# Optimization experiments

Hardware: AMD Instinct MI355X
Metric: run time of the kernel (lower is better)

Reference implementation:

```python
import jax, jax.numpy as jnp
import numpy as np

B, N, H, D = 4, 2048, 16, 64
FEATS = H * D  # 1024; module scales scores by sqrt(feats), not sqrt(head_dim)


def setup_inputs() -> dict:
    key = jax.random.key(0)
    ks = jax.random.split(key, 9)
    s = 1.0 / np.sqrt(D)
    return {
        "x": jax.random.normal(ks[0], (B, N, H, D), dtype=jnp.float32),
        "Wq": jax.random.uniform(ks[1], (H, D, D), jnp.float32, -s, s),
        "bq": jax.random.uniform(ks[2], (H, D), jnp.float32, -s, s),
        "Wk": jax.random.uniform(ks[3], (H, D, D), jnp.float32, -s, s),
        "bk": jax.random.uniform(ks[4], (H, D), jnp.float32, -s, s),
        "Wv": jax.random.uniform(ks[5], (H, D, D), jnp.float32, -s, s),
        "bv": jax.random.uniform(ks[6], (H, D), jnp.float32, -s, s),
        "Wo": jax.random.uniform(ks[7], (H, D, D), jnp.float32, -s, s),
        "bo": jax.random.uniform(ks[8], (H, D), jnp.float32, -s, s),
    }


def reference(x, Wq, bq, Wk, bk, Wv, bv, Wo, bo):
    # per-head linears as one batched einsum: [b,n,h,d] x [h,d,o] -> [b,n,h,o]
    q = jnp.einsum("bnhd,hdo->bnho", x, Wq) + bq
    k = jnp.einsum("bnhd,hdo->bnho", x, Wk) + bk
    v = jnp.einsum("bnhd,hdo->bnho", x, Wv) + bv
    sqrt_d = jnp.asarray(FEATS, x.dtype) ** 0.5  # sqrt(feats) per original code
    # scores: [b,h,i,j]
    score = jax.nn.softmax(jnp.einsum("bihf,bjhf->bhij", q, k) / sqrt_d, axis=-1)
    attn = jnp.einsum("bhij,bjhf->bihf", score, v)  # [b,n,h,d]
    out = jnp.einsum("bnhd,hdo->bnho", attn, Wo) + bo
    return out
```

## Files before the change

kernel.cpp:

```cpp
#include <hip/hip_runtime.h>

#define Bsz  4
#define Nseq 2048
#define Hn   16
#define Dh   64
#define BH   (Bsz*Hn)
#define NT64 (Nseq/64)
#define NT32 (Nseq/32)

#define AS1 __attribute__((address_space(1)))
#define AS3 __attribute__((address_space(3)))

typedef __attribute__((ext_vector_type(8))) short bf16x8;
typedef __attribute__((ext_vector_type(16))) float f32x16;
typedef __attribute__((ext_vector_type(4))) float f32x4;
typedef __attribute__((ext_vector_type(2))) float f32x2;
typedef __attribute__((ext_vector_type(4))) unsigned short u16x4;

#define MFMA32 __builtin_amdgcn_mfma_f32_32x32x16_bf16

static __device__ __forceinline__ unsigned short f2bf(float f) {
    unsigned u = __float_as_uint(f);
    u = (u + 0x7fffu + ((u >> 16) & 1u)) >> 16;
    return (unsigned short)u;
}
static __device__ __forceinline__ float bf2f(unsigned short s) {
    return __uint_as_float((unsigned)s << 16);
}
static __device__ __forceinline__ unsigned cvt_pk_bf16(float lo, float hi) {
    unsigned r;
    asm("v_cvt_pk_bf16_f32 %0, %1, %2" : "=v"(r) : "v"(lo), "v"(hi));
    return r;
}
static __device__ __forceinline__ void swap32(unsigned &a, unsigned &b) {
    asm("v_permlane32_swap_b32 %0, %1" : "+v"(a), "+v"(b));
}
static __device__ __forceinline__ float exp2v(float x) {
    float r;
    asm("v_exp_f32 %0, %1" : "=v"(r) : "v"(x));
    return r;
}
static __device__ __forceinline__ f32x2 pk_add(f32x2 a, f32x2 b) {
    f32x2 d;
    asm("v_pk_add_f32 %0, %1, %2" : "=v"(d) : "v"(a), "v"(b));
    return d;
}

__global__ __launch_bounds__(256) void wprep_kernel(
    const float* __restrict__ Wq, const float* __restrict__ Wk,
    const float* __restrict__ Wv,
    unsigned short* __restrict__ gWtH, unsigned short* __restrict__ gWtL)
{
    __shared__ float ws[64][65];
    const int mh = blockIdx.x;
    const int m = mh >> 4, h = mh & 15;
    const int tid = threadIdx.x;
    const float* W = (m == 0 ? Wq : (m == 1 ? Wk : Wv)) + h * 4096;

    for (int c = tid; c < 1024; c += 256) {
        int row = c >> 4, col = (c & 15) * 4;
        *(f32x4*)&ws[row][col] = *(const f32x4*)&W[row * 64 + col];
    }
    __syncthreads();

    const int o = tid >> 2, dblk = (tid & 3) * 16;
    size_t base = ((size_t)mh * 64 + o) * 64 + dblk;
#pragma unroll
    for (int i4 = 0; i4 < 4; ++i4) {
        u16x4 vh, vl;
#pragma unroll
        for (int j = 0; j < 4; ++j) {
            float v = ws[dblk + i4 * 4 + j][o];
            unsigned short hh = f2bf(v);
            vh[j] = hh;
            vl[j] = f2bf(v - bf2f(hh));
        }
        *(u16x4*)&gWtH[base + i4 * 4] = vh;
        *(u16x4*)&gWtL[base + i4 * 4] = vl;
    }
}

__global__ __launch_bounds__(256) void proj_kernel(
    const float* __restrict__ x,
    const unsigned short* __restrict__ gWtH, const unsigned short* __restrict__ gWtL,
    const float* __restrict__ bq, const float* __restrict__ bk,
    const float* __restrict__ bv,
    unsigned short* __restrict__ gQ, unsigned short* __restrict__ gK,
    unsigned short* __restrict__ gVt)
{
    const int bh = blockIdx.x, h = bh & (Hn - 1), b = bh >> 4;
    const int n0 = blockIdx.y * 64;
    const int tid = threadIdx.x;
    const int w = tid >> 6, lane = tid & 63, l31 = lane & 31, l5 = lane >> 5;
    const int qi = w >> 1, oj = w & 1;

    const int nrow = n0 + qi * 32 + l31;
    const float* xrow = x + (((size_t)b * Nseq + nrow) * Hn + h) * Dh;

    bf16x8 xh[4], xl[4];
#pragma unroll
    for (int ks = 0; ks < 4; ++ks) {
        f32x4 v0 = *(const f32x4*)&xrow[ks * 16 + l5 * 8];
        f32x4 v1 = *(const f32x4*)&xrow[ks * 16 + l5 * 8 + 4];
#pragma unroll
        for (int e = 0; e < 4; ++e) {
            unsigned short h0 = f2bf(v0[e]);
            xh[ks][e] = (short)h0;
            xl[ks][e] = (short)f2bf(v0[e] - bf2f(h0));
            unsigned short h1 = f2bf(v1[e]);
            xh[ks][4 + e] = (short)h1;
            xl[ks][4 + e] = (short)f2bf(v1[e] - bf2f(h1));
        }
    }

    const int o = oj * 32 + l31;

    f32x16 acc[3] = {};
#pragma unroll
    for (int m = 0; m < 3; ++m) {
        const unsigned short* WH = gWtH + (((size_t)m * 16 + h) * 64 + o) * 64;
        const unsigned short* WL = gWtL + (((size_t)m * 16 + h) * 64 + o) * 64;
#pragma unroll
        for (int ks = 0; ks < 4; ++ks) {
            bf16x8 wh = *(const bf16x8*)&WH[ks * 16 + l5 * 8];
            bf16x8 wl = *(const bf16x8*)&WL[ks * 16 + l5 * 8];
            if (m < 2) {
                acc[m] = MFMA32(xh[ks], wh, acc[m], 0, 0, 0);
                acc[m] = MFMA32(xl[ks], wh, acc[m], 0, 0, 0);
                acc[m] = MFMA32(xh[ks], wl, acc[m], 0, 0, 0);
            } else {
                acc[2] = MFMA32(wh, xh[ks], acc[2], 0, 0, 0);
                acc[2] = MFMA32(wl, xh[ks], acc[2], 0, 0, 0);
                acc[2] = MFMA32(wh, xl[ks], acc[2], 0, 0, 0);
            }
        }
    }

    {
        float bias = bq[h * 64 + o];
#pragma unroll
        for (int r = 0; r < 16; ++r) {
            int nl = (r & 3) + 8 * (r >> 2) + 4 * l5;
            int n = n0 + qi * 32 + nl;
            gQ[((size_t)bh * Nseq + n) * Dh + o] =
                f2bf((acc[0][r] + bias) * 0.0450842200f);
        }
    }
    {
        float bias = bk[h * 64 + o];
#pragma unroll
        for (int r = 0; r < 16; ++r) {
            int nl = (r & 3) + 8 * (r >> 2) + 4 * l5;
            int n = n0 + qi * 32 + nl;
            int c = (((o >> 3) ^ (n & 7)) * 8) + (o & 7);
            gK[((size_t)bh * Nseq + n) * Dh + c] = f2bf(acc[1][r] + bias);
        }
    }
    {
        const int tile = (n0 >> 5) + qi;
        const int kt = l31;
#pragma unroll
        for (int r = 0; r < 16; ++r) {
            int ol = (r & 3) + 8 * (r >> 2) + 4 * l5;
            int ov = oj * 32 + ol;
            float bias = bv[h * 64 + ov];
            int c = (((kt >> 3) ^ ((ov >> 2) & 3)) * 8) + (kt & 7);
            gVt[(((size_t)bh * NT32 + tile) * 64 + ov) * 32 + c] =
                f2bf(acc[2][r] + bias);
        }
    }
}

__global__ __launch_bounds__(256, 4) void flash_kernel(
    const unsigned short* __restrict__ gQ,
    const unsigned short* __restrict__ gK,
    const unsigned short* __restrict__ gVt,
    const float* __restrict__ Wo, const float* __restrict__ bo,
    float* __restrict__ out)
{
    __shared__ unsigned short kbuf[2][4096];
    __shared__ unsigned short vbuf[2][4096];

    const int bh = blockIdx.x, h = bh & (Hn - 1), b = bh >> 4;
    const int tid = threadIdx.x;
    const int w = tid >> 6, lane = tid & 63;
    const int l31 = lane & 31, l5 = lane >> 5;
    const int qrow = blockIdx.y * 128 + w * 32 + l31;

    bf16x8 qf[4];
#pragma unroll
    for (int kk = 0; kk < 4; ++kk)
        qf[kk] = *(const bf16x8*)&gQ[((size_t)bh * Nseq + qrow) * Dh + kk * 16 + l5 * 8];

    float z0 = 0.f;
    asm volatile("" : "+v"(z0));
    f32x16 zc = {z0, z0, z0, z0, z0, z0, z0, z0, z0, z0, z0, z0, z0, z0, z0, z0};

    f32x16 acc[2] = {};
    float l = 0.f;

    auto stage = [&](int t, int bufi) {
        const unsigned short* ks = gK + ((size_t)bh * Nseq + (size_t)t * 64) * Dh;
        const unsigned short* vs = gVt + ((size_t)(bh * NT32 + 2 * t)) * 2048;
#pragma unroll
        for (int i = 0; i < 2; ++i) {
            int off = w * 1024 + i * 512 + lane * 8;
            __builtin_amdgcn_global_load_lds((const AS1 void*)(ks + off),
                                             (AS3 void*)(&kbuf[bufi][w * 1024 + i * 512]), 16, 0, 0);
            __builtin_amdgcn_global_load_lds((const AS1 void*)(vs + off),
                                             (AS3 void*)(&vbuf[bufi][w * 1024 + i * 512]), 16, 0, 0);
        }
    };

    auto qk_tile = [&](const unsigned short* __restrict__ kb) -> f32x16 {
        const int roff = l31 * 64;
        const int sw = l31 & 7;
        bf16x8 kf = *(const bf16x8*)&kb[roff + ((l5 ^ sw) * 8)];
        f32x16 s = MFMA32(kf, qf[0], zc, 0, 0, 0);
#pragma unroll
        for (int kk = 1; kk < 4; ++kk) {
            kf = *(const bf16x8*)&kb[roff + (((kk * 2 + l5) ^ sw) * 8)];
            s = MFMA32(kf, qf[kk], s, 0, 0, 0);
        }
        return s;
    };

    auto soft_pv = [&](f32x16& s, const unsigned short* __restrict__ vb) {
#pragma unroll
        for (int r = 0; r < 16; ++r) s[r] = exp2v(s[r]);
        f32x2* sp = (f32x2*)&s;
        f32x2 u0 = pk_add(sp[0], sp[1]), u1 = pk_add(sp[2], sp[3]);
        f32x2 u2 = pk_add(sp[4], sp[5]), u3 = pk_add(sp[6], sp[7]);
        u0 = pk_add(u0, u1); u2 = pk_add(u2, u3);
        u0 = pk_add(u0, u2);
        l += u0[0] + u0[1];
#pragma unroll
        for (int ks = 0; ks < 2; ++ks) {
            const int b0 = 8 * ks;
            unsigned x0 = cvt_pk_bf16(s[b0 + 0], s[b0 + 1]);
            unsigned x1 = cvt_pk_bf16(s[b0 + 2], s[b0 + 3]);
            unsigned y0 = cvt_pk_bf16(s[b0 + 4], s[b0 + 5]);
            unsigned y1 = cvt_pk_bf16(s[b0 + 6], s[b0 + 7]);
            swap32(x0, y0);
            swap32(x1, y1);
            bf16x8 pf;
            ((unsigned*)&pf)[0] = x0; ((unsigned*)&pf)[1] = x1;
            ((unsigned*)&pf)[2] = y0; ((unsigned*)&pf)[3] = y1;
#pragma unroll
            for (int dt = 0; dt < 2; ++dt) {
                const int row = dt * 32 + l31;
                bf16x8 vf = *(const bf16x8*)&vb[row * 32 + (((ks * 2 + l5) ^ ((row >> 2) & 3)) * 8)];
                acc[dt] = MFMA32(vf, pf, acc[dt], 0, 0, 0);
            }
        }
    };

    auto window_step = [&](const unsigned short* __restrict__ kb,
                           const unsigned short* __restrict__ vb) {
        f32x16 sA = qk_tile(kb);
        f32x16 sB = qk_tile(kb + 2048);
        soft_pv(sA, vb);
        soft_pv(sB, vb + 2048);
    };

    stage(0, 0);

#pragma unroll 1
    for (int t2 = 0; t2 < NT64; t2 += 2) {
        __syncthreads();
        stage(t2 + 1, 1);
        window_step(&kbuf[0][0], &vbuf[0][0]);
        __syncthreads();
        if (t2 + 2 < NT64) stage(t2 + 2, 0);
        window_step(&kbuf[1][0], &vbuf[1][0]);
    }

    __syncthreads();
    {
        unsigned short* wl = &kbuf[0][0];
        for (int c = tid; c < 512; c += 256) {
            int o = c >> 3, c8 = c & 7;
            int cc = ((c8 ^ (o & 7)) * 8);
#pragma unroll
            for (int jj = 0; jj < 4; ++jj) wl[o * 64 + cc + jj]     = f2bf(Wo[(h * 64 + c8 * 8 + jj) * 64 + o]);
#pragma unroll
            for (int jj = 0; jj < 4; ++jj) wl[o * 64 + cc + 4 + jj] = f2bf(Wo[(h * 64 + c8 * 8 + 4 + jj) * 64 + o]);
        }
    }
    __syncthreads();

    l += __shfl_xor(l, 32);
    float inv = 1.f / l;
#pragma unroll
    for (int dt = 0; dt < 2; ++dt)
#pragma unroll
        for (int r = 0; r < 16; ++r) acc[dt][r] *= inv;

    const unsigned short* wot = &kbuf[0][0];
    f32x16 oc[2] = {};
#pragma unroll
    for (int kk = 0; kk < 4; ++kk) {
        const int dt = kk >> 1;
        const int b0 = 8 * (kk & 1);
        unsigned x0 = cvt_pk_bf16(acc[dt][b0 + 0], acc[dt][b0 + 1]);
        unsigned x1 = cvt_pk_bf16(acc[dt][b0 + 2], acc[dt][b0 + 3]);
        unsigned y0 = cvt_pk_bf16(acc[dt][b0 + 4], acc[dt][b0 + 5]);
        unsigned y1 = cvt_pk_bf16(acc[dt][b0 + 6], acc[dt][b0 + 7]);
        swap32(x0, y0);
        swap32(x1, y1);
        bf16x8 af;
        ((unsigned*)&af)[0] = x0; ((unsigned*)&af)[1] = x1;
        ((unsigned*)&af)[2] = y0; ((unsigned*)&af)[3] = y1;
#pragma unroll
        for (int ot = 0; ot < 2; ++ot) {
            int row = ot * 32 + l31;
            bf16x8 wf = *(const bf16x8*)&wot[row * 64 + (((kk * 2 + l5) ^ (row & 7)) * 8)];
            oc[ot] = MFMA32(wf, af, oc[ot], 0, 0, 0);
        }
    }

    float* obase = out + (((size_t)b * Nseq + qrow) * Hn + h) * Dh;
#pragma unroll
    for (int ot = 0; ot < 2; ++ot)
#pragma unroll
        for (int rq = 0; rq < 4; ++rq) {
            int o = ot * 32 + rq * 8 + l5 * 4;
            f32x4 bb = *(const f32x4*)&bo[h * 64 + o];
            f32x4 vv;
            vv[0] = oc[ot][rq * 4 + 0] + bb[0];
            vv[1] = oc[ot][rq * 4 + 1] + bb[1];
            vv[2] = oc[ot][rq * 4 + 2] + bb[2];
            vv[3] = oc[ot][rq * 4 + 3] + bb[3];
            *(f32x4*)&obase[o] = vv;
        }
}

extern "C" void kernel_launch(void* const* d_in, const int* in_sizes, int n_in,
                              void* d_out, int out_size, void* d_ws, size_t ws_size,
                              hipStream_t stream) {
    const float* x  = (const float*)d_in[0];
    const float* Wq = (const float*)d_in[1];
    const float* bq = (const float*)d_in[2];
    const float* Wk = (const float*)d_in[3];
    const float* bk = (const float*)d_in[4];
    const float* Wv = (const float*)d_in[5];
    const float* bv = (const float*)d_in[6];
    const float* Wo = (const float*)d_in[7];
    const float* bo = (const float*)d_in[8];
    float* out = (float*)d_out;

    unsigned short* gQ   = (unsigned short*)d_ws;
    unsigned short* gK   = gQ + (size_t)BH * Nseq * Dh;
    unsigned short* gVt  = gK + (size_t)BH * Nseq * Dh;
    unsigned short* gWtH = gVt + (size_t)BH * Nseq * Dh;
    unsigned short* gWtL = gWtH + (size_t)3 * 16 * 64 * 64;

    wprep_kernel<<<48, 256, 0, stream>>>(Wq, Wk, Wv, gWtH, gWtL);
    proj_kernel<<<dim3(BH, Nseq / 64), 256, 0, stream>>>(x, gWtH, gWtL, bq, bk, bv, gQ, gK, gVt);
    flash_kernel<<<dim3(BH, Nseq / 128), 256, 0, stream>>>(gQ, gK, gVt, Wo, bo, out);
}
```

Before: 126.2 us.

## Stage projection outputs through LDS for coalesced stores; precompute LDS addresses and set MFMA priority

The projection kernel now writes Q, K and V tiles into a shared staging buffer and then stores them to global memory as 16-byte vectors, instead of scattered 2-byte stores. This aims to cut uncoalesced global write traffic, at the cost of extra barriers and LDS usage. The flash kernel precomputes swizzled LDS base pointers once, so address arithmetic leaves the inner loop. It also raises wave priority around the MFMA blocks with s_setprio, aiming for better overlap between waves.

New measurement: 130.3 us. +3.2%, slower.

```diff
diff --git a/kernel.cpp b/kernel.cpp
--- a/kernel.cpp
+++ b/kernel.cpp
@@ -88,6 +88,8 @@
     unsigned short* __restrict__ gQ, unsigned short* __restrict__ gK,
     unsigned short* __restrict__ gVt)
 {
+    __shared__ unsigned short st[64][72];
+
     const int bh = blockIdx.x, h = bh & (Hn - 1), b = bh >> 4;
     const int n0 = blockIdx.y * 64;
     const int tid = threadIdx.x;
@@ -136,38 +138,61 @@
         }
     }
 
+    const size_t gbase = (size_t)bh * Nseq + n0;
+
     {
         float bias = bq[h * 64 + o];
 #pragma unroll
         for (int r = 0; r < 16; ++r) {
             int nl = (r & 3) + 8 * (r >> 2) + 4 * l5;
-            int n = n0 + qi * 32 + nl;
-            gQ[((size_t)bh * Nseq + n) * Dh + o] =
-                f2bf((acc[0][r] + bias) * 0.0450842200f);
-        }
-    }
+            st[qi * 32 + nl][o] = f2bf((acc[0][r] + bias) * 0.0450842200f);
+        }
+    }
+    __syncthreads();
+#pragma unroll
+    for (int i = 0; i < 2; ++i) {
+        int c = i * 256 + tid;
+        int row = c >> 3, ch = c & 7;
+        bf16x8 v = *(const bf16x8*)&st[row][ch * 8];
+        *(bf16x8*)&gQ[(gbase + row) * Dh + ch * 8] = v;
+    }
+    __syncthreads();
+
     {
         float bias = bk[h * 64 + o];
 #pragma unroll
         for (int r = 0; r < 16; ++r) {
             int nl = (r & 3) + 8 * (r >> 2) + 4 * l5;
-            int n = n0 + qi * 32 + nl;
-            int c = (((o >> 3) ^ (n & 7)) * 8) + (o & 7);
-            gK[((size_t)bh * Nseq + n) * Dh + c] = f2bf(acc[1][r] + bias);
-        }
-    }
+            st[qi * 32 + nl][o] = f2bf(acc[1][r] + bias);
+        }
+    }
+    __syncthreads();
+#pragma unroll
+    for (int i = 0; i < 2; ++i) {
+        int c = i * 256 + tid;
+        int row = c >> 3, ch = c & 7;
+        bf16x8 v = *(const bf16x8*)&st[row][ch * 8];
+        *(bf16x8*)&gK[(gbase + row) * Dh + ((ch ^ (row & 7)) * 8)] = v;
+    }
+    __syncthreads();
+
     {
-        const int tile = (n0 >> 5) + qi;
-        const int kt = l31;
 #pragma unroll
         for (int r = 0; r < 16; ++r) {
             int ol = (r & 3) + 8 * (r >> 2) + 4 * l5;
             int ov = oj * 32 + ol;
-            float bias = bv[h * 64 + ov];
-            int c = (((kt >> 3) ^ ((ov >> 2) & 3)) * 8) + (kt & 7);
-            gVt[(((size_t)bh * NT32 + tile) * 64 + ov) * 32 + c] =
-                f2bf(acc[2][r] + bias);
-        }
+            st[ov][qi * 32 + l31] = f2bf(acc[2][r] + bv[h * 64 + ov]);
+        }
+    }
+    __syncthreads();
+#pragma unroll
+    for (int i = 0; i < 2; ++i) {
+        int c = i * 256 + tid;
+        int orow = c >> 3, ch = c & 7;
+        int tile = ch >> 2, c4 = ch & 3;
+        bf16x8 v = *(const bf16x8*)&st[orow][ch * 8];
+        *(bf16x8*)&gVt[((size_t)(bh * NT32 + (n0 >> 5) + tile)) * 2048 +
+                       orow * 32 + ((c4 ^ ((orow >> 2) & 3)) * 8)] = v;
     }
 }
 
@@ -192,6 +217,15 @@
     for (int kk = 0; kk < 4; ++kk)
         qf[kk] = *(const bf16x8*)&gQ[((size_t)bh * Nseq + qrow) * Dh + kk * 16 + l5 * 8];
 
+    const unsigned short* kbase[4];
+#pragma unroll
+    for (int kk = 0; kk < 4; ++kk)
+        kbase[kk] = &kbuf[0][l31 * 64 + (((kk * 2 + l5) ^ (l31 & 7)) * 8)];
+    const unsigned short* vbase[2];
+#pragma unroll
+    for (int ks = 0; ks < 2; ++ks)
+        vbase[ks] = &vbuf[0][l31 * 32 + (((ks * 2 + l5) ^ ((l31 >> 2) & 3)) * 8)];
+
     float z0 = 0.f;
     asm volatile("" : "+v"(z0));
     f32x16 zc = {z0, z0, z0, z0, z0, z0, z0, z0, z0, z0, z0, z0, z0, z0, z0, z0};
@@ -212,20 +246,7 @@
         }
     };
 
-    auto qk_tile = [&](const unsigned short* __restrict__ kb) -> f32x16 {
-        const int roff = l31 * 64;
-        const int sw = l31 & 7;
-        bf16x8 kf = *(const bf16x8*)&kb[roff + ((l5 ^ sw) * 8)];
-        f32x16 s = MFMA32(kf, qf[0], zc, 0, 0, 0);
-#pragma unroll
-        for (int kk = 1; kk < 4; ++kk) {
-            kf = *(const bf16x8*)&kb[roff + (((kk * 2 + l5) ^ sw) * 8)];
-            s = MFMA32(kf, qf[kk], s, 0, 0, 0);
-        }
-        return s;
-    };
-
-    auto soft_pv = [&](f32x16& s, const unsigned short* __restrict__ vb) {
+    auto soft_pv = [&](f32x16& s, const int sub, const int buf) {
 #pragma unroll
         for (int r = 0; r < 16; ++r) s[r] = exp2v(s[r]);
         f32x2* sp = (f32x2*)&s;
@@ -246,21 +267,40 @@
             bf16x8 pf;
             ((unsigned*)&pf)[0] = x0; ((unsigned*)&pf)[1] = x1;
             ((unsigned*)&pf)[2] = y0; ((unsigned*)&pf)[3] = y1;
+            __builtin_amdgcn_s_setprio(1);
 #pragma unroll
             for (int dt = 0; dt < 2; ++dt) {
-                const int row = dt * 32 + l31;
-                bf16x8 vf = *(const bf16x8*)&vb[row * 32 + (((ks * 2 + l5) ^ ((row >> 2) & 3)) * 8)];
+                bf16x8 vf = *(const bf16x8*)(vbase[ks] + dt * 1024 + sub * 2048 + buf * 4096);
                 acc[dt] = MFMA32(vf, pf, acc[dt], 0, 0, 0);
             }
+            __builtin_amdgcn_s_setprio(0);
         }
     };
 
-    auto window_step = [&](const unsigned short* __restrict__ kb,
-                           const unsigned short* __restrict__ vb) {
-        f32x16 sA = qk_tile(kb);
-        f32x16 sB = qk_tile(kb + 2048);
-        soft_pv(sA, vb);
-        soft_pv(sB, vb + 2048);
+    auto window = [&](const int buf) {
+        f32x16 sA, sB;
+        __builtin_amdgcn_s_setprio(1);
+        {
+            bf16x8 kf = *(const bf16x8*)(kbase[0] + buf * 4096);
+            sA = MFMA32(kf, qf[0], zc, 0, 0, 0);
+            kf = *(const bf16x8*)(kbase[1] + buf * 4096);
+            sA = MFMA32(kf, qf[1], sA, 0, 0, 0);
+            kf = *(const bf16x8*)(kbase[2] + buf * 4096);
+            sA = MFMA32(kf, qf[2], sA, 0, 0, 0);
+            kf = *(const bf16x8*)(kbase[3] + buf * 4096);
+            sA = MFMA32(kf, qf[3], sA, 0, 0, 0);
+            kf = *(const bf16x8*)(kbase[0] + 2048 + buf * 4096);
+            sB = MFMA32(kf, qf[0], zc, 0, 0, 0);
+            kf = *(const bf16x8*)(kbase[1] + 2048 + buf * 4096);
+            sB = MFMA32(kf, qf[1], sB, 0, 0, 0);
+            kf = *(const bf16x8*)(kbase[2] + 2048 + buf * 4096);
+            sB = MFMA32(kf, qf[2], sB, 0, 0, 0);
+            kf = *(const bf16x8*)(kbase[3] + 2048 + buf * 4096);
+            sB = MFMA32(kf, qf[3], sB, 0, 0, 0);
+        }
+        __builtin_amdgcn_s_setprio(0);
+        soft_pv(sA, 0, buf);
+        soft_pv(sB, 1, buf);
     };
 
     stage(0, 0);
@@ -269,10 +309,10 @@
     for (int t2 = 0; t2 < NT64; t2 += 2) {
         __syncthreads();
         stage(t2 + 1, 1);
-        window_step(&kbuf[0][0], &vbuf[0][0]);
+        window(0);
         __syncthreads();
         if (t2 + 2 < NT64) stage(t2 + 2, 0);
-        window_step(&kbuf[1][0], &vbuf[1][0]);
+        window(1);
     }
 
     __syncthreads();
@@ -296,7 +336,6 @@
 #pragma unroll
         for (int r = 0; r < 16; ++r) acc[dt][r] *= inv;
 
-    const unsigned short* wot = &kbuf[0][0];
     f32x16 oc[2] = {};
 #pragma unroll
     for (int kk = 0; kk < 4; ++kk) {
@@ -313,8 +352,7 @@
         ((unsigned*)&af)[2] = y0; ((unsigned*)&af)[3] = y1;
 #pragma unroll
         for (int ot = 0; ot < 2; ++ot) {
-            int row = ot * 32 + l31;
-            bf16x8 wf = *(const bf16x8*)&wot[row * 64 + (((kk * 2 + l5) ^ (row & 7)) * 8)];
+            bf16x8 wf = *(const bf16x8*)(kbase[kk] + ot * 2048);
             oc[ot] = MFMA32(wf, af, oc[ot], 0, 0, 0);
         }
     }
```
